# Optimization experiments

Hardware: AMD Instinct MI355X
Metric: run time of the kernel (lower is better)

The kernel has to match this reference:

```python
import jax, jax.numpy as jnp
import numpy as np

N = 1_000_000   # number of scattered items
D = 256         # in_embed_dim == key_proj_dim
E = 100_000     # nr_elements (number of segments)


def setup_inputs() -> dict:
    key = jax.random.key(0)
    k1, k2, k3, k4, k5 = jax.random.split(key, 5)
    bound = 1.0 / np.sqrt(D)
    scattered_values = jax.random.normal(k1, (N, D), dtype=jnp.float32)
    indices = jax.random.randint(k2, (N,), 0, E, dtype=jnp.int32)
    # key projection Linear(D, D) params (PyTorch default-style init)
    W_key = jax.random.uniform(k3, (D, D), minval=-bound, maxval=bound, dtype=jnp.float32)
    b_key = jax.random.uniform(k4, (D,), minval=-bound, maxval=bound, dtype=jnp.float32)
    # general_attention_weight ~ U(-1/sqrt(key_proj_dim), +)
    attn_w = jax.random.uniform(k5, (D,), minval=-bound, maxval=bound, dtype=jnp.float32)
    return {
        "scattered_values": scattered_values,
        "indices": indices,
        "nr_elements": E,
        "W_key": W_key,
        "b_key": b_key,
        "attn_w": attn_w,
    }


def reference(scattered_values, indices, nr_elements, W_key, b_key, attn_w):
    # key projection: [N, D]
    keys = scattered_values @ W_key.T + b_key
    # general attention logits, scaled: [N]
    probs = (keys @ attn_w) * (D ** -0.5)
    # scatter_softmax over segments (stable: subtract per-segment max)
    seg_max = jax.ops.segment_max(probs, indices, num_segments=nr_elements)
    seg_max = jnp.where(jnp.isfinite(seg_max), seg_max, 0.0)  # empty segments
    ex = jnp.exp(probs - seg_max[indices])
    denom = jax.ops.segment_sum(ex, indices, num_segments=nr_elements)
    scores = ex / denom[indices]
    # weighted scatter-sum of (unprojected) values: [E, D]
    attn_applied = jax.ops.segment_sum(
        scattered_values * scores[:, None], indices, num_segments=nr_elements
    )
    return scores, attn_applied
```

## Files before the change

### kernel.cpp

```cpp
#include <hip/hip_runtime.h>


#define DIM 256
#define WAVE 64

__global__ void compute_w_kernel(const float* __restrict__ W,
                                 const float* __restrict__ b,
                                 const float* __restrict__ a,
                                 float* __restrict__ wc) {
    const int k = blockIdx.x, j = threadIdx.x;
    __shared__ float sm[256];
    sm[j] = (k < DIM) ? a[j] * W[j * DIM + k] : a[j] * b[j];
    __syncthreads();
    for (int d = 128; d; d >>= 1) {
        if (j < d) sm[j] += sm[j + d];
        __syncthreads();
    }
    if (j == 0) wc[k] = sm[0];
}

__global__ void rank_kernel(const int* __restrict__ idx,
                            int* __restrict__ counts,
                            int* __restrict__ rank, int n) {
    const int i = blockIdx.x * 256 + threadIdx.x;
    if (i < n) rank[i] = atomicAdd(&counts[idx[i]], 1);
}

__global__ void scan1_kernel(const int* __restrict__ counts,
                             int* __restrict__ offsets,
                             int* __restrict__ bsums, int e) {
    __shared__ int s[256];
    const int t = threadIdx.x, g = blockIdx.x * 256 + t;
    const int x = (g < e) ? counts[g] : 0;
    s[t] = x; __syncthreads();
    for (int d = 1; d < 256; d <<= 1) {
        const int v = (t >= d) ? s[t - d] : 0; __syncthreads();
        s[t] += v; __syncthreads();
    }
    if (g < e) offsets[g] = s[t] - x;
    if (t == 255) bsums[blockIdx.x] = s[255];
}

__global__ void scan2_kernel(int* __restrict__ bsums, int nb) {
    __shared__ int s[512];
    const int t = threadIdx.x;
    const int x = (t < nb) ? bsums[t] : 0;
    s[t] = x; __syncthreads();
    for (int d = 1; d < 512; d <<= 1) {
        const int v = (t >= d) ? s[t - d] : 0; __syncthreads();
        s[t] += v; __syncthreads();
    }
    if (t < nb) bsums[t] = s[t] - x;
}

__global__ void scan3_kernel(int* __restrict__ offsets,
                             const int* __restrict__ bsums, int e, int n) {
    const int g = blockIdx.x * 256 + threadIdx.x;
    if (g < e) offsets[g] += bsums[blockIdx.x];
    if (g == 0) offsets[e] = n;
}

__global__ void scatter_kernel(const int* __restrict__ idx,
                               const int* __restrict__ rank,
                               const int* __restrict__ offsets,
                               int* __restrict__ perm, int n) {
    const int i = blockIdx.x * 256 + threadIdx.x;
    if (i < n) perm[offsets[idx[i]] + rank[i]] = i;
}

__global__ void seg_fused_kernel(const float4* __restrict__ v4,
                                 const int* __restrict__ perm,
                                 const float* __restrict__ wc,
                                 const int* __restrict__ offsets,
                                 float* __restrict__ scores,
                                 float* __restrict__ attn, int e) {
    const int lane = threadIdx.x & (WAVE - 1);
    const int s = (blockIdx.x * blockDim.x + threadIdx.x) >> 6;
    if (s >= e) return;
    const float4 wf = ((const float4*)wc)[lane];
    const float c = wc[DIM];
    const int base = offsets[s];
    const int cnt  = offsets[s + 1] - base;
    float4 acc = make_float4(0.f, 0.f, 0.f, 0.f);

    if (cnt > 0 && cnt <= WAVE) {
        const int i_l = (lane < cnt) ? perm[base + lane] : 0;
        float myp = 0.f, d = 0.f;
        #pragma unroll
        for (int ch = 0; ch < 8; ++ch) {
            const int st = ch * 8;
            if (st < cnt) {
                int ix8[8];
                #pragma unroll
                for (int t = 0; t < 8; ++t) ix8[t] = __shfl(i_l, st + t, WAVE);
                float4 row8[8];
                #pragma unroll
                for (int t = 0; t < 8; ++t)
                    if (st + t < cnt)
                        row8[t] = v4[(size_t)ix8[t] * (DIM / 4) + lane];
                #pragma unroll
                for (int t = 0; t < 8; ++t) {
                    if (st + t < cnt) {
                        float pp = row8[t].x * wf.x + row8[t].y * wf.y
                                 + row8[t].z * wf.z + row8[t].w * wf.w;
                        #pragma unroll
                        for (int off = 32; off; off >>= 1)
                            pp += __shfl_xor(pp, off, WAVE);
                        const float pe = __expf((pp + c) * 0.0625f);
                        d += pe;
                        acc.x += pe * row8[t].x; acc.y += pe * row8[t].y;
                        acc.z += pe * row8[t].z; acc.w += pe * row8[t].w;
                        if (lane == st + t) myp = pe;
                    }
                }
            }
        }
        const float inv = 1.f / d;
        if (lane < cnt) scores[i_l] = myp * inv;
        acc.x *= inv; acc.y *= inv; acc.z *= inv; acc.w *= inv;
    } else if (cnt > WAVE) {
        float d = 0.f;
        for (int t = 0; t < cnt; ++t) {
            const int i = perm[base + t];
            const float4 vv = v4[(size_t)i * (DIM / 4) + lane];
            float pp = vv.x * wf.x + vv.y * wf.y + vv.z * wf.z + vv.w * wf.w;
            #pragma unroll
            for (int off = 32; off; off >>= 1) pp += __shfl_xor(pp, off, WAVE);
            const float pe = __expf((pp + c) * 0.0625f);
            d += pe;
            acc.x += pe * vv.x; acc.y += pe * vv.y;
            acc.z += pe * vv.z; acc.w += pe * vv.w;
        }
        const float inv = 1.f / d;
        for (int t = 0; t < cnt; ++t) {
            const int i = perm[base + t];
            const float4 vv = v4[(size_t)i * (DIM / 4) + lane];
            float pp = vv.x * wf.x + vv.y * wf.y + vv.z * wf.z + vv.w * wf.w;
            #pragma unroll
            for (int off = 32; off; off >>= 1) pp += __shfl_xor(pp, off, WAVE);
            if (lane == 0) scores[i] = __expf((pp + c) * 0.0625f) * inv;
        }
        acc.x *= inv; acc.y *= inv; acc.z *= inv; acc.w *= inv;
    }
    ((float4*)(attn + (size_t)s * DIM))[lane] = acc;
}

extern "C" void kernel_launch(void* const* d_in, const int* in_sizes, int n_in,
                              void* d_out, int out_size, void* d_ws, size_t ws_size,
                              hipStream_t stream) {
    const float* v   = (const float*)d_in[0];
    const int*   idx = (const int*)d_in[1];
    const float* W   = (const float*)d_in[3];
    const float* b   = (const float*)d_in[4];
    const float* a   = (const float*)d_in[5];

    const int n = in_sizes[0] / DIM;
    const int e = (out_size - n) / DIM;
    const int nb = (e + 255) / 256;

    float* scores = (float*)d_out;
    float* attn   = (float*)d_out + n;

    float* wc      = (float*)d_ws;
    int*   counts  = (int*)(wc + 512);
    int*   offsets = counts + e;
    int*   bsums   = offsets + e + 2;
    int*   rank    = bsums + 512;
    int*   perm    = rank + n;

    hipMemsetAsync(counts, 0, (size_t)e * sizeof(int), stream);
    compute_w_kernel<<<DIM + 1, 256, 0, stream>>>(W, b, a, wc);

    rank_kernel<<<(n + 255) / 256, 256, 0, stream>>>(idx, counts, rank, n);
    scan1_kernel<<<nb, 256, 0, stream>>>(counts, offsets, bsums, e);
    scan2_kernel<<<1, 512, 0, stream>>>(bsums, nb);
    scan3_kernel<<<nb, 256, 0, stream>>>(offsets, bsums, e, n);
    scatter_kernel<<<(n + 255) / 256, 256, 0, stream>>>(idx, rank, offsets, perm, n);

    seg_fused_kernel<<<(e + 3) / 4, 256, 0, stream>>>((const float4*)v, perm, wc,
                                                      offsets, scores, attn, e);
}
```

Measured before the change: 317.1 us.

## Double-buffer segment row loads, use nontemporal loads/stores, merge weight and rank kernels

The segment kernel now prefetches the next chunk of eight gathered rows while computing on the current chunk, and loops only over the chunks actually needed. Row loads and output stores use nontemporal builtins. The weight-folding and rank-counting kernels are merged into one launch to save a launch and let the two pieces overlap. Prefetching doubles the per-lane row registers, which may lower occupancy.

```diff
diff --git a/kernel.cpp b/kernel.cpp
--- a/kernel.cpp
+++ b/kernel.cpp
@@ -4,26 +4,30 @@
 #define DIM 256
 #define WAVE 64
 
-__global__ void compute_w_kernel(const float* __restrict__ W,
-                                 const float* __restrict__ b,
-                                 const float* __restrict__ a,
-                                 float* __restrict__ wc) {
-    const int k = blockIdx.x, j = threadIdx.x;
-    __shared__ float sm[256];
-    sm[j] = (k < DIM) ? a[j] * W[j * DIM + k] : a[j] * b[j];
-    __syncthreads();
-    for (int d = 128; d; d >>= 1) {
-        if (j < d) sm[j] += sm[j + d];
+typedef float f4 __attribute__((ext_vector_type(4)));
+
+__global__ void cw_rank_kernel(const float* __restrict__ W,
+                               const float* __restrict__ b,
+                               const float* __restrict__ a,
+                               float* __restrict__ wc,
+                               const int* __restrict__ idx,
+                               int* __restrict__ counts,
+                               int* __restrict__ rank, int n) {
+    const int t = threadIdx.x;
+    if (blockIdx.x <= DIM) {
+        const int k = blockIdx.x;
+        __shared__ float sm[256];
+        sm[t] = (k < DIM) ? a[t] * W[t * DIM + k] : a[t] * b[t];
         __syncthreads();
+        for (int d = 128; d; d >>= 1) {
+            if (t < d) sm[t] += sm[t + d];
+            __syncthreads();
+        }
+        if (t == 0) wc[k] = sm[0];
+    } else {
+        const int i = (blockIdx.x - DIM - 1) * 256 + t;
+        if (i < n) rank[i] = atomicAdd(&counts[idx[i]], 1);
     }
-    if (j == 0) wc[k] = sm[0];
-}
-
-__global__ void rank_kernel(const int* __restrict__ idx,
-                            int* __restrict__ counts,
-                            int* __restrict__ rank, int n) {
-    const int i = blockIdx.x * 256 + threadIdx.x;
-    if (i < n) rank[i] = atomicAdd(&counts[idx[i]], 1);
 }
 
 __global__ void scan1_kernel(const int* __restrict__ counts,
@@ -68,7 +72,7 @@
     if (i < n) perm[offsets[idx[i]] + rank[i]] = i;
 }
 
-__global__ void seg_fused_kernel(const float4* __restrict__ v4,
+__global__ void seg_fused_kernel(const f4* __restrict__ v4,
                                  const int* __restrict__ perm,
                                  const float* __restrict__ wc,
                                  const int* __restrict__ offsets,
@@ -77,43 +81,49 @@
     const int lane = threadIdx.x & (WAVE - 1);
     const int s = (blockIdx.x * blockDim.x + threadIdx.x) >> 6;
     if (s >= e) return;
-    const float4 wf = ((const float4*)wc)[lane];
+    const f4 wf = ((const f4*)wc)[lane];
     const float c = wc[DIM];
     const int base = offsets[s];
     const int cnt  = offsets[s + 1] - base;
-    float4 acc = make_float4(0.f, 0.f, 0.f, 0.f);
+    f4 acc = {0.f, 0.f, 0.f, 0.f};
 
     if (cnt > 0 && cnt <= WAVE) {
         const int i_l = (lane < cnt) ? perm[base + lane] : 0;
         float myp = 0.f, d = 0.f;
+        const int nch = (cnt + 7) >> 3;
+        f4 cur[8], nxt[8];
         #pragma unroll
-        for (int ch = 0; ch < 8; ++ch) {
+        for (int t = 0; t < 8; ++t)
+            if (t < cnt)
+                cur[t] = __builtin_nontemporal_load(
+                    v4 + (size_t)__shfl(i_l, t, WAVE) * (DIM / 4) + lane);
+        for (int ch = 0; ch < nch; ++ch) {
             const int st = ch * 8;
-            if (st < cnt) {
-                int ix8[8];
-                #pragma unroll
-                for (int t = 0; t < 8; ++t) ix8[t] = __shfl(i_l, st + t, WAVE);
-                float4 row8[8];
+            if (ch + 1 < nch) {
+                const int st2 = st + 8;
                 #pragma unroll
                 for (int t = 0; t < 8; ++t)
-                    if (st + t < cnt)
-                        row8[t] = v4[(size_t)ix8[t] * (DIM / 4) + lane];
-                #pragma unroll
-                for (int t = 0; t < 8; ++t) {
-                    if (st + t < cnt) {
-                        float pp = row8[t].x * wf.x + row8[t].y * wf.y
-                                 + row8[t].z * wf.z + row8[t].w * wf.w;
-                        #pragma unroll
-                        for (int off = 32; off; off >>= 1)
-                            pp += __shfl_xor(pp, off, WAVE);
-                        const float pe = __expf((pp + c) * 0.0625f);
-                        d += pe;
-                        acc.x += pe * row8[t].x; acc.y += pe * row8[t].y;
-                        acc.z += pe * row8[t].z; acc.w += pe * row8[t].w;
-                        if (lane == st + t) myp = pe;
-                    }
+                    if (st2 + t < cnt)
+                        nxt[t] = __builtin_nontemporal_load(
+                            v4 + (size_t)__shfl(i_l, st2 + t, WAVE) * (DIM / 4) + lane);
+            }
+            #pragma unroll
+            for (int t = 0; t < 8; ++t) {
+                if (st + t < cnt) {
+                    float pp = cur[t].x * wf.x + cur[t].y * wf.y
+                             + cur[t].z * wf.z + cur[t].w * wf.w;
+                    #pragma unroll
+                    for (int off = 32; off; off >>= 1)
+                        pp += __shfl_xor(pp, off, WAVE);
+                    const float pe = __expf((pp + c) * 0.0625f);
+                    d += pe;
+                    acc.x += pe * cur[t].x; acc.y += pe * cur[t].y;
+                    acc.z += pe * cur[t].z; acc.w += pe * cur[t].w;
+                    if (lane == st + t) myp = pe;
                 }
             }
+            #pragma unroll
+            for (int t = 0; t < 8; ++t) cur[t] = nxt[t];
         }
         const float inv = 1.f / d;
         if (lane < cnt) scores[i_l] = myp * inv;
@@ -122,7 +132,7 @@
         float d = 0.f;
         for (int t = 0; t < cnt; ++t) {
             const int i = perm[base + t];
-            const float4 vv = v4[(size_t)i * (DIM / 4) + lane];
+            const f4 vv = v4[(size_t)i * (DIM / 4) + lane];
             float pp = vv.x * wf.x + vv.y * wf.y + vv.z * wf.z + vv.w * wf.w;
             #pragma unroll
             for (int off = 32; off; off >>= 1) pp += __shfl_xor(pp, off, WAVE);
@@ -134,7 +144,7 @@
         const float inv = 1.f / d;
         for (int t = 0; t < cnt; ++t) {
             const int i = perm[base + t];
-            const float4 vv = v4[(size_t)i * (DIM / 4) + lane];
+            const f4 vv = v4[(size_t)i * (DIM / 4) + lane];
             float pp = vv.x * wf.x + vv.y * wf.y + vv.z * wf.z + vv.w * wf.w;
             #pragma unroll
             for (int off = 32; off; off >>= 1) pp += __shfl_xor(pp, off, WAVE);
@@ -142,7 +152,7 @@
         }
         acc.x *= inv; acc.y *= inv; acc.z *= inv; acc.w *= inv;
     }
-    ((float4*)(attn + (size_t)s * DIM))[lane] = acc;
+    __builtin_nontemporal_store(acc, (f4*)(attn + (size_t)s * DIM) + lane);
 }
 
 extern "C" void kernel_launch(void* const* d_in, const int* in_sizes, int n_in,
@@ -169,14 +179,13 @@
     int*   perm    = rank + n;
 
     hipMemsetAsync(counts, 0, (size_t)e * sizeof(int), stream);
-    compute_w_kernel<<<DIM + 1, 256, 0, stream>>>(W, b, a, wc);
-
-    rank_kernel<<<(n + 255) / 256, 256, 0, stream>>>(idx, counts, rank, n);
+    cw_rank_kernel<<<DIM + 1 + (n + 255) / 256, 256, 0, stream>>>(
+        W, b, a, wc, idx, counts, rank, n);
     scan1_kernel<<<nb, 256, 0, stream>>>(counts, offsets, bsums, e);
     scan2_kernel<<<1, 512, 0, stream>>>(bsums, nb);
     scan3_kernel<<<nb, 256, 0, stream>>>(offsets, bsums, e, n);
     scatter_kernel<<<(n + 255) / 256, 256, 0, stream>>>(idx, rank, offsets, perm, n);
 
-    seg_fused_kernel<<<(e + 3) / 4, 256, 0, stream>>>((const float4*)v, perm, wc,
+    seg_fused_kernel<<<(e + 3) / 4, 256, 0, stream>>>((const f4*)v, perm, wc,
                                                       offsets, scores, attn, e);
 }
```

Measured after the change: 284.1 us (median of 2 runs). 10.4% less time.
